# Optimization experiments

Measured on AMD Instinct MI355X. Metric: run time of the kernel, lower is better.

## Reference

```python
import jax, jax.numpy as jnp
import numpy as np

LAMBDA = 25.0
MU = 25.0
NU = 1.0
ALPHA = 0.25
EPS = 1e-4
NUM_MATCHES = (20, 4)


def _cdist(x, y):
    # x: (B, L1, C), y: (B, L2, C) -> (B, L1, L2) euclidean distances
    x2 = jnp.sum(x * x, axis=-1)[..., :, None]
    y2 = jnp.sum(y * y, axis=-1)[..., None, :]
    d2 = x2 + y2 - 2.0 * jnp.einsum('blc,bmc->blm', x, y)
    return jnp.sqrt(jnp.maximum(d2, 0.0))


def _nearest_neighbors(input_maps, candidate_maps, distances, num_matches):
    # For each input location, its nearest candidate; then keep the
    # num_matches input locations with smallest NN distance, in original order.
    nn_dist = jnp.min(distances, axis=-1)    # (B, L1)
    nn_idx = jnp.argmin(distances, axis=-1)  # (B, L1)
    _, sel = jax.lax.top_k(-nn_dist, num_matches)  # (B, M) smallest distances
    sel = jnp.sort(sel, axis=1)  # restore original ordering of positions
    filtered_input = jnp.take_along_axis(input_maps, sel[..., None], axis=1)
    nn_sel = jnp.take_along_axis(nn_idx, sel, axis=1)
    filtered_candidate = jnp.take_along_axis(candidate_maps, nn_sel[..., None], axis=1)
    return filtered_input, filtered_candidate


def _mse(a, b):
    return jnp.mean((a - b) ** 2)


def _vicreg_loss(z_a, z_b):
    inv_loss = _mse(z_a, z_b)

    def var_loss(z):
        std = jnp.sqrt(jnp.var(z, axis=0, ddof=1) + EPS)
        return jnp.mean(jax.nn.relu(1.0 - std))

    def cov_loss(z):
        n, d = z.shape
        zc = z - jnp.mean(z, axis=0)
        cov = (zc.T @ zc) / (n - 1)
        off = cov - jnp.diag(jnp.diag(cov))
        return jnp.sum(off ** 2) / d

    v = 0.5 * (var_loss(z_a) + var_loss(z_b))
    c = cov_loss(z_a) + cov_loss(z_b)
    return LAMBDA * inv_loss + MU * v + NU * c


def _local_loss(z_global, z_local, grid_global, grid_local):
    B = z_global.shape[0]
    zg = z_global.reshape(B, -1, z_global.shape[-1])   # (B, Lg, C)
    zl = z_local.reshape(B, -1, z_local.shape[-1])     # (B, Ll, C)

    inv_loss = 0.0
    # feature-space NN
    gf, gn = _nearest_neighbors(zg, zl, _cdist(zg, zl), NUM_MATCHES[0])
    lf, ln = _nearest_neighbors(zl, zg, _cdist(zl, zg), NUM_MATCHES[1])
    inv_loss = inv_loss + (_mse(gf, gn) / 2 + _mse(lf, ln) / 2)

    # grid-space NN (distances from grids, gather from feature maps)
    gg = grid_global.reshape(B, -1, 2)
    gl = grid_local.reshape(B, -1, 2)
    gf, gn = _nearest_neighbors(zg, zl, _cdist(gg, gl), NUM_MATCHES[0])
    lf, ln = _nearest_neighbors(zl, zg, _cdist(gl, gg), NUM_MATCHES[1])
    inv_loss = inv_loss + (_mse(gf, gn) / 2 + _mse(lf, ln) / 2)

    return LAMBDA * inv_loss


def setup_inputs() -> dict:
    key = jax.random.key(0)
    ks = jax.random.split(key, 6)
    B, D, C = 32, 8192, 512
    return {
        'z_global': jax.random.normal(ks[0], (B, D), jnp.float32),
        'z_local': jax.random.normal(ks[1], (B, D), jnp.float32),
        'z_global_local_features': jax.random.normal(ks[2], (B, 24, 24, C), jnp.float32),
        'z_local_local_features': jax.random.normal(ks[3], (B, 16, 16, C), jnp.float32),
        'grid_global': jax.random.uniform(ks[4], (B, 24, 24, 2), jnp.float32),
        'grid_local': jax.random.uniform(ks[5], (B, 16, 16, 2), jnp.float32),
    }


def reference(z_global, z_local, z_global_local_features, z_local_local_features, grid_global, grid_local):
    global_loss = _vicreg_loss(z_global, z_local)
    local_loss = _local_loss(z_global_local_features, z_local_local_features, grid_global, grid_local)
    return ALPHA * global_loss + (1.0 - ALPHA) * local_loss
```

## Files before the change

kernel.cpp:

```cpp
#include <hip/hip_runtime.h>
#include <hip/hip_bf16.h>

#define BATCH 32
#define DZ    8192
#define LG    576
#define LL    256
#define CH    512

#define OFF_S      0
#define OFF_BSUM   8192
#define OFF_SELSUM 9472
#define OFF_CNT    10496
#define OFF_RNP    10560
#define OFF_CNP    305472
#define WS_NEED    895296

typedef __attribute__((ext_vector_type(8))) short bf16x8;
typedef __attribute__((ext_vector_type(4))) float f32x4;

__device__ __forceinline__ unsigned short f2bf(float x) {
  union { __hip_bfloat16 h; unsigned short u; } cv;
  cv.h = __float2bfloat16(x);
  return cv.u;
}

__device__ __forceinline__ uint4 pack8(float4 lo, float4 hi) {
  union { unsigned short h[8]; uint4 u; } pk;
  pk.h[0] = f2bf(lo.x); pk.h[1] = f2bf(lo.y); pk.h[2] = f2bf(lo.z); pk.h[3] = f2bf(lo.w);
  pk.h[4] = f2bf(hi.x); pk.h[5] = f2bf(hi.y); pk.h[6] = f2bf(hi.z); pk.h[7] = f2bf(hi.w);
  return pk.u;
}

__device__ __forceinline__ float dot4(float4 v) {
  return v.x * v.x + v.y * v.y + v.z * v.z + v.w * v.w;
}

struct SelSmem {
  unsigned long long keys[LG];
  unsigned int nnm[LG];
  float cxy[2 * LG];
  unsigned int plist[40];
  unsigned int cnt;
  float fred[4];
};

template <int V>
__device__ __forceinline__ void sel_case(
    SelSmem& sm, int b,
    const float* __restrict__ zgf, const float* __restrict__ zlf,
    const float* __restrict__ gg, const float* __restrict__ gl,
    const unsigned long long* __restrict__ rowNNp,
    const unsigned long long* __restrict__ colNNp,
    double* __restrict__ selsum) {
  constexpr bool GDIR = (V == 0 || V == 2);
  constexpr int L1 = GDIR ? LG : LL;
  constexpr int L2 = GDIR ? LL : LG;
  constexpr int M  = GDIR ? 20 : 4;
  constexpr int NR = (L1 + 255) / 256;
  const float* fin  = GDIR ? zgf + (size_t)b * LG * CH : zlf + (size_t)b * LL * CH;
  const float* fcan = GDIR ? zlf + (size_t)b * LL * CH : zgf + (size_t)b * LG * CH;
  int tid = threadIdx.x, lane = tid & 63, wv = tid >> 6;
  if (tid == 0) sm.cnt = 0;

  if constexpr (V < 2) {
    constexpr int P = (V == 0) ? 2 : 9;
    const unsigned long long* src =
        (V == 0) ? rowNNp + (size_t)b * LG * 2 : colNNp + (size_t)b * LL * 9;
    #pragma unroll
    for (int s = 0; s < NR; ++s) {
      int l = tid + s * 256;
      if (l < L1) {
        const unsigned long long* q = src + (size_t)l * P;
        unsigned long long p = q[0];
        #pragma unroll
        for (int u = 1; u < P; ++u) { unsigned long long t2 = q[u]; p = t2 < p ? t2 : p; }
        sm.keys[l] = (p & 0xFFFFFFFF00000000ull) | (unsigned)l;
        sm.nnm[l] = (unsigned)(p & 0xFFFFFFFFu);
      }
    }
  } else {
    const float* gin  = (V == 2) ? gg + (size_t)b * LG * 2 : gl + (size_t)b * LL * 2;
    const float* gcan = (V == 2) ? gl + (size_t)b * LL * 2 : gg + (size_t)b * LG * 2;
    #pragma unroll
    for (int s = 0; s < (2 * L2 + 255) / 256; ++s) {
      int i = tid + s * 256;
      if (i < 2 * L2) sm.cxy[i] = gcan[i];
    }
    __syncthreads();
    float x[NR], y[NR], bd[NR];
    unsigned bi[NR];
    #pragma unroll
    for (int s = 0; s < NR; ++s) {
      int l = tid + s * 256;
      x[s] = (l < L1) ? gin[2 * l] : 0.f;
      y[s] = (l < L1) ? gin[2 * l + 1] : 0.f;
      bd[s] = 3.4e38f; bi[s] = 0;
    }
    const float2* c2 = (const float2*)sm.cxy;
    for (int m2 = 0; m2 < L2; m2 += 8) {
      float2 cc[8];
      #pragma unroll
      for (int u = 0; u < 8; ++u) cc[u] = c2[m2 + u];
      #pragma unroll
      for (int u = 0; u < 8; ++u)
        #pragma unroll
        for (int s = 0; s < NR; ++s) {
          float dx = x[s] - cc[u].x, dy = y[s] - cc[u].y;
          float d2 = dx * dx + dy * dy;
          if (d2 < bd[s]) { bd[s] = d2; bi[s] = (unsigned)(m2 + u); }
        }
    }
    #pragma unroll
    for (int s = 0; s < NR; ++s) {
      int l = tid + s * 256;
      if (l < L1) {
        sm.keys[l] = ((unsigned long long)__float_as_uint(bd[s]) << 32) | (unsigned)l;
        sm.nnm[l] = bi[s];
      }
    }
  }
  __syncthreads();

  unsigned long long myk[NR];
  int rk[NR];
  #pragma unroll
  for (int s = 0; s < NR; ++s) {
    int l = tid + s * 256;
    myk[s] = (l < L1) ? sm.keys[l] : ~0ull;
    rk[s] = 0;
  }
  for (int j = 0; j < L1; j += 8) {
    unsigned long long kk[8];
    #pragma unroll
    for (int u = 0; u < 8; ++u) kk[u] = sm.keys[j + u];
    #pragma unroll
    for (int u = 0; u < 8; ++u)
      #pragma unroll
      for (int s = 0; s < NR; ++s) rk[s] += (kk[u] < myk[s]) ? 1 : 0;
  }
  #pragma unroll
  for (int s = 0; s < NR; ++s) {
    int l = tid + s * 256;
    if (l < L1 && rk[s] < M) {
      unsigned slot = atomicAdd(&sm.cnt, 1u);
      sm.plist[2 * slot] = (unsigned)l;
      sm.plist[2 * slot + 1] = sm.nnm[l];
    }
  }
  __syncthreads();

  float part = 0.f;
  #pragma unroll
  for (int rr = 0; rr < M / 4; ++rr) {
    int r = wv + rr * 4;
    const float4* a4 = (const float4*)(fin + (size_t)sm.plist[2 * r] * CH);
    const float4* c4 = (const float4*)(fcan + (size_t)sm.plist[2 * r + 1] * CH);
    float4 xa = a4[lane * 2], xb = a4[lane * 2 + 1];
    float4 ya = c4[lane * 2], yb = c4[lane * 2 + 1];
    float d0 = xa.x - ya.x, d1 = xa.y - ya.y, d2 = xa.z - ya.z, d3 = xa.w - ya.w;
    float d4 = xb.x - yb.x, d5 = xb.y - yb.y, d6 = xb.z - yb.z, d7 = xb.w - yb.w;
    part += d0 * d0 + d1 * d1 + d2 * d2 + d3 * d3 +
            d4 * d4 + d5 * d5 + d6 * d6 + d7 * d7;
  }
  for (int s = 32; s; s >>= 1) part += __shfl_down(part, s);
  if (lane == 0) sm.fred[wv] = part;
  __syncthreads();
  if (tid == 0)
    selsum[V * 32 + b] = (double)(sm.fred[0] + sm.fred[1] + sm.fred[2] + sm.fred[3]);
}

__global__ __launch_bounds__(256) void k_megaA(
    const float* __restrict__ za, const float* __restrict__ zb,
    const float* __restrict__ zgf, const float* __restrict__ zlf,
    const float* __restrict__ gg, const float* __restrict__ gl,
    double* __restrict__ bsum, float* __restrict__ S,
    unsigned long long* __restrict__ rowNNp, unsigned long long* __restrict__ colNNp,
    double* __restrict__ selsum, unsigned int* __restrict__ cnt) {
  __shared__ __align__(16) char smem[31488];
  int tid = threadIdx.x, lane = tid & 63, wv = tid >> 6;
  int blk = blockIdx.x;

  if (blk < 64) {
    SelSmem& sm = *reinterpret_cast<SelSmem*>(smem);
    int b2 = blk >> 1;
    if (blk & 1) sel_case<3>(sm, b2, zgf, zlf, gg, gl, rowNNp, colNNp, selsum);
    else         sel_case<2>(sm, b2, zgf, zlf, gg, gl, rowNNp, colNNp, selsum);
    return;
  }

  if (blk < 640) {
    int fblk = blk - 64;
    int fs = (fblk & 7) * 72 + (fblk >> 3);
    int b = fs / 18, rr_ = fs % 18;
    int by = rr_ / 9, bx = rr_ % 9;
    int row0 = bx * 64, col0 = by * 128;

    unsigned short (*As0)[40] = (unsigned short(*)[40])smem;
    unsigned short (*Bs0)[40] = (unsigned short(*)[40])(smem + 5120);
    unsigned short (*As1)[40] = (unsigned short(*)[40])(smem + 15360);
    unsigned short (*Bs1)[40] = (unsigned short(*)[40])(smem + 20480);
    float* Asn = (float*)(smem + 30720);
    float* Bsn = (float*)(smem + 30976);

    const int m16 = lane & 15, quad = lane >> 4;
    const int wm = wv >> 1, wn = wv & 1;
    const float* Ag = zgf + ((size_t)(b * LG + row0)) * CH;
    const float* Bg = zlf + ((size_t)(b * LL + col0)) * CH;
    const int sr = tid >> 2, sq = tid & 3;
    const int br = tid >> 1, bq = tid & 1;

    f32x4 acc[2][4] = {};
    float ssA = 0.f, ssB = 0.f;
    float4 a0, a1, b0, b1, b2, b3;

    const float* apb = Ag + (size_t)sr * CH + sq * 8;
    const float* bpb = Bg + (size_t)br * CH + bq * 16;

    a0 = *(const float4*)(apb);     a1 = *(const float4*)(apb + 4);
    b0 = *(const float4*)(bpb);     b1 = *(const float4*)(bpb + 4);
    b2 = *(const float4*)(bpb + 8); b3 = *(const float4*)(bpb + 12);
    *(uint4*)&As0[sr][sq * 8]       = pack8(a0, a1);
    *(uint4*)&Bs0[br][bq * 16]      = pack8(b0, b1);
    *(uint4*)&Bs0[br][bq * 16 + 8]  = pack8(b2, b3);
    ssA += dot4(a0) + dot4(a1);
    ssB += dot4(b0) + dot4(b1) + dot4(b2) + dot4(b3);
    a0 = *(const float4*)(apb + 32);      a1 = *(const float4*)(apb + 36);
    b0 = *(const float4*)(bpb + 32);      b1 = *(const float4*)(bpb + 36);
    b2 = *(const float4*)(bpb + 40);      b3 = *(const float4*)(bpb + 44);
    __syncthreads();

    #pragma unroll
    for (int k = 0; k < 8; ++k) {
      {
        bf16x8 af0 = *(const bf16x8*)&As0[wm * 32 + m16][quad * 8];
        bf16x8 af1 = *(const bf16x8*)&As0[wm * 32 + 16 + m16][quad * 8];
        bf16x8 bfv[4];
        #pragma unroll
        for (int j = 0; j < 4; ++j)
          bfv[j] = *(const bf16x8*)&Bs0[wn * 64 + j * 16 + m16][quad * 8];
        #pragma unroll
        for (int j = 0; j < 4; ++j) {
          acc[0][j] = __builtin_amdgcn_mfma_f32_16x16x32_bf16(af0, bfv[j], acc[0][j], 0, 0, 0);
          acc[1][j] = __builtin_amdgcn_mfma_f32_16x16x32_bf16(af1, bfv[j], acc[1][j], 0, 0, 0);
        }
        *(uint4*)&As1[sr][sq * 8]      = pack8(a0, a1);
        *(uint4*)&Bs1[br][bq * 16]     = pack8(b0, b1);
        *(uint4*)&Bs1[br][bq * 16 + 8] = pack8(b2, b3);
        ssA += dot4(a0) + dot4(a1);
        ssB += dot4(b0) + dot4(b1) + dot4(b2) + dot4(b3);
        if (k < 7) {
          int k0 = (2 * k + 2) * 32;
          a0 = *(const float4*)(apb + k0);      a1 = *(const float4*)(apb + k0 + 4);
          b0 = *(const float4*)(bpb + k0);      b1 = *(const float4*)(bpb + k0 + 4);
          b2 = *(const float4*)(bpb + k0 + 8);  b3 = *(const float4*)(bpb + k0 + 12);
        }
        __syncthreads();
      }
      {
        bf16x8 af0 = *(const bf16x8*)&As1[wm * 32 + m16][quad * 8];
        bf16x8 af1 = *(const bf16x8*)&As1[wm * 32 + 16 + m16][quad * 8];
        bf16x8 bfv[4];
        #pragma unroll
        for (int j = 0; j < 4; ++j)
          bfv[j] = *(const bf16x8*)&Bs1[wn * 64 + j * 16 + m16][quad * 8];
        #pragma unroll
        for (int j = 0; j < 4; ++j) {
          acc[0][j] = __builtin_amdgcn_mfma_f32_16x16x32_bf16(af0, bfv[j], acc[0][j], 0, 0, 0);
          acc[1][j] = __builtin_amdgcn_mfma_f32_16x16x32_bf16(af1, bfv[j], acc[1][j], 0, 0, 0);
        }
        if (k < 7) {
          *(uint4*)&As0[sr][sq * 8]      = pack8(a0, a1);
          *(uint4*)&Bs0[br][bq * 16]     = pack8(b0, b1);
          *(uint4*)&Bs0[br][bq * 16 + 8] = pack8(b2, b3);
          ssA += dot4(a0) + dot4(a1);
          ssB += dot4(b0) + dot4(b1) + dot4(b2) + dot4(b3);
          int k0 = (2 * k + 3) * 32;
          a0 = *(const float4*)(apb + k0);      a1 = *(const float4*)(apb + k0 + 4);
          b0 = *(const float4*)(bpb + k0);      b1 = *(const float4*)(bpb + k0 + 4);
          b2 = *(const float4*)(bpb + k0 + 8);  b3 = *(const float4*)(bpb + k0 + 12);
          __syncthreads();
        }
      }
    }

    ssA += __shfl_xor(ssA, 1); ssA += __shfl_xor(ssA, 2);
    ssB += __shfl_xor(ssB, 1);
    __syncthreads();
    if (sq == 0) Asn[sr] = ssA;
    if (bq == 0) Bsn[br] = ssB;
    __syncthreads();

    float na[2][4], nb[4];
    #pragma unroll
    for (int i = 0; i < 2; ++i)
      #pragma unroll
      for (int r = 0; r < 4; ++r)
        na[i][r] = Asn[wm * 32 + i * 16 + quad * 4 + r];
    #pragma unroll
    for (int j = 0; j < 4; ++j)
      nb[j] = Bsn[wn * 64 + j * 16 + m16];

    #pragma unroll
    for (int i = 0; i < 2; ++i) {
      #pragma unroll
      for (int r = 0; r < 4; ++r) {
        unsigned long long p = ~0ull;
        #pragma unroll
        for (int j = 0; j < 4; ++j) {
          float d = fmaxf(na[i][r] + nb[j] - 2.f * acc[i][j][r], 0.f);
          unsigned c = (unsigned)(col0 + wn * 64 + j * 16 + m16);
          unsigned long long pj = (((unsigned long long)__float_as_uint(d)) << 32) | c;
          p = pj < p ? pj : p;
        }
        #pragma unroll
        for (int s = 1; s < 16; s <<= 1) {
          unsigned long long q = __shfl_xor(p, s);
          p = q < p ? q : p;
        }
        if (m16 == 0)
          rowNNp[((size_t)b * LG + row0 + wm * 32 + i * 16 + quad * 4 + r) * 2 + by] = p;
      }
    }
    #pragma unroll
    for (int j = 0; j < 4; ++j) {
      unsigned long long p = ~0ull;
      #pragma unroll
      for (int i = 0; i < 2; ++i) {
        #pragma unroll
        for (int r = 0; r < 4; ++r) {
          float d = fmaxf(na[i][r] + nb[j] - 2.f * acc[i][j][r], 0.f);
          unsigned rg = (unsigned)(row0 + wm * 32 + i * 16 + quad * 4 + r);
          unsigned long long pr = (((unsigned long long)__float_as_uint(d)) << 32) | rg;
          p = pr < p ? pr : p;
        }
      }
      unsigned long long q = __shfl_xor(p, 16); p = q < p ? q : p;
      q = __shfl_xor(p, 32); p = q < p ? q : p;
      if (quad == 0)
        colNNp[((size_t)b * LL + col0 + wn * 64 + j * 16 + m16) * 9 + bx] = p;
    }
    return;
  }

  if (blk < 1696) {
    float (*sred)[5] = (float(*)[5])smem;
    int e = blk - 640;
    int zi = e >= 528; if (zi) e -= 528;
    const float* z = zi ? zb : za;
    float* Sz = S + zi * 1024;
    int p = 0, rem = e;
    while (rem >= 32 - p) { rem -= 32 - p; ++p; }
    int q = p + rem;
    const float4* zp = (const float4*)(z + (size_t)p * DZ);
    const float4* zq = (const float4*)(z + (size_t)q * DZ);
    float s = 0.f;
    #pragma unroll
    for (int ii = 0; ii < 8; ++ii) {
      int i = tid + ii * 256;
      float4 a = zp[i], bb = zq[i];
      s += a.x * bb.x + a.y * bb.y + a.z * bb.z + a.w * bb.w;
    }
    for (int off = 32; off; off >>= 1) s += __shfl_down(s, off);
    if (lane == 0) sred[wv][0] = s;
    __syncthreads();
    if (tid == 0) {
      float r = sred[0][0] + sred[1][0] + sred[2][0] + sred[3][0];
      Sz[p * 32 + q] = r;
      if (p != q) Sz[q * 32 + p] = r;
    }
    return;
  }

  {
    float (*sred)[5] = (float(*)[5])smem;
    int blkS = blk - 1696;
    if (blkS == 0 && tid == 0) cnt[0] = 0;
    int i = blkS * 256 + tid;
    float sa = 0.f, qa = 0.f, sb = 0.f, qb = 0.f, si = 0.f;
    #pragma unroll 8
    for (int b = 0; b < BATCH; ++b) {
      float va = za[(size_t)b * DZ + i];
      float vb = zb[(size_t)b * DZ + i];
      sa += va; qa += va * va;
      sb += vb; qb += vb * vb;
      float d = va - vb; si += d * d;
    }
    float ssa = qa - sa * sa * (1.f / 32.f);
    float ssb = qb - sb * sb * (1.f / 32.f);
    float v0 = si;
    float v1 = fmaxf(0.f, 1.f - sqrtf(ssa * (1.f / 31.f) + 1e-4f));
    float v2 = fmaxf(0.f, 1.f - sqrtf(ssb * (1.f / 31.f) + 1e-4f));
    float v3 = ssa * ssa, v4 = ssb * ssb;
    for (int off = 32; off; off >>= 1) {
      v0 += __shfl_down(v0, off); v1 += __shfl_down(v1, off);
      v2 += __shfl_down(v2, off); v3 += __shfl_down(v3, off);
      v4 += __shfl_down(v4, off);
    }
    if (lane == 0) {
      sred[wv][0] = v0; sred[wv][1] = v1; sred[wv][2] = v2;
      sred[wv][3] = v3; sred[wv][4] = v4;
    }
    __syncthreads();
    if (tid < 5)
      bsum[blkS * 5 + tid] =
          (double)(sred[0][tid] + sred[1][tid] + sred[2][tid] + sred[3][tid]);
  }
}

struct TailSmem {
  SelSmem sel;
  float t[2][32];
  double sacc[5];
  double smf[4];
  int isLast;
};

__global__ __launch_bounds__(256) void k_tail(
    const float* __restrict__ zgf, const float* __restrict__ zlf,
    const float* __restrict__ gg, const float* __restrict__ gl,
    const unsigned long long* __restrict__ rowNNp,
    const unsigned long long* __restrict__ colNNp,
    double* __restrict__ selsum, const double* __restrict__ bsum,
    const float* __restrict__ S, unsigned int* __restrict__ doneCnt,
    float* __restrict__ out) {
  __shared__ TailSmem ts;
  int tid = threadIdx.x;
  int b = blockIdx.x >> 1, V = blockIdx.x & 1;
  if (V == 0) sel_case<0>(ts.sel, b, zgf, zlf, gg, gl, rowNNp, colNNp, selsum);
  else        sel_case<1>(ts.sel, b, zgf, zlf, gg, gl, rowNNp, colNNp, selsum);

  if (tid == 0) {
    __threadfence();
    unsigned r = atomicAdd(doneCnt, 1u);
    ts.isLast = (r == 63) ? 1 : 0;
  }
  __syncthreads();
  if (!ts.isLast) return;
  __threadfence();

  if (tid < 32) {
    #pragma unroll
    for (int zi = 0; zi < 2; ++zi) {
      float tp = 0.f;
      for (int bb = 0; bb < 32; ++bb) tp += S[zi * 1024 + tid * 32 + bb];
      ts.t[zi][tid] = tp * (1.f / 32.f);
    }
  }
  if (tid < 5) {
    double s = 0.0;
    for (int blk2 = 0; blk2 < 32; ++blk2) s += bsum[blk2 * 5 + tid];
    ts.sacc[tid] = s;
  }
  if (tid >= 8 && tid < 12) {
    int v = tid - 8;
    double s = 0.0;
    for (int bb = 0; bb < 32; ++bb) s += selsum[v * 32 + bb];
    ts.smf[v] = s;
  }
  __syncthreads();
  if (tid < 64) {
    double total[2];
    #pragma unroll
    for (int zi = 0; zi < 2; ++zi) {
      float u = 0.f;
      for (int bb = 0; bb < 32; ++bb) u += ts.t[zi][bb];
      u *= (1.f / 32.f);
      double s = 0.0;
      for (int e2 = tid; e2 < 1024; e2 += 64) {
        int p = e2 >> 5, q = e2 & 31;
        float G = S[zi * 1024 + e2] - ts.t[zi][p] - ts.t[zi][q] + u;
        s += (double)G * (double)G;
      }
      for (int off = 32; off; off >>= 1) s += __shfl_down(s, off);
      total[zi] = s;
    }
    if (tid == 0) {
      double inv_g = ts.sacc[0] / (32.0 * 8192.0);
      double v = 0.5 * (ts.sacc[1] + ts.sacc[2]) / 8192.0;
      double c = (total[0] - ts.sacc[3] + total[1] - ts.sacc[4]) / (961.0 * 8192.0);
      double gloss = 25.0 * inv_g + 25.0 * v + c;
      double mfg = ts.smf[0] / (32.0 * 20.0 * 512.0);
      double mfl = ts.smf[1] / (32.0 * 4.0 * 512.0);
      double mgg = ts.smf[2] / (32.0 * 20.0 * 512.0);
      double mgl = ts.smf[3] / (32.0 * 4.0 * 512.0);
      double lloss = 25.0 * (0.5 * (mfg + mfl) + 0.5 * (mgg + mgl));
      out[0] = (float)(0.25 * gloss + 0.75 * lloss);
    }
  }
}

extern "C" void kernel_launch(void* const* d_in, const int* in_sizes, int n_in,
                              void* d_out, int out_size, void* d_ws, size_t ws_size,
                              hipStream_t stream) {
  const float* zg  = (const float*)d_in[0];
  const float* zl  = (const float*)d_in[1];
  const float* zgf = (const float*)d_in[2];
  const float* zlf = (const float*)d_in[3];
  const float* gg  = (const float*)d_in[4];
  const float* glo = (const float*)d_in[5];

  char* ws = (char*)d_ws;
  float* S       = (float*)(ws + OFF_S);
  double* bsum   = (double*)(ws + OFF_BSUM);
  double* selsum = (double*)(ws + OFF_SELSUM);
  unsigned int* cnt = (unsigned int*)(ws + OFF_CNT);
  unsigned long long* rowNNp = (unsigned long long*)(ws + OFF_RNP);
  unsigned long long* colNNp = (unsigned long long*)(ws + OFF_CNP);

  k_megaA<<<1728, 256, 0, stream>>>(zg, zl, zgf, zlf, gg, glo,
                                    bsum, S, rowNNp, colNNp, selsum, cnt);
  k_tail<<<64, 256, 0, stream>>>(zgf, zlf, gg, glo, rowNNp, colNNp,
                                 selsum, bsum, S, cnt, (float*)d_out);
}
```

Baseline: 137.9 us.

## Fuse per-batch feature-NN selection into distance blocks via last-block counters

The feature-space NN selection (sel_case 0/1) moves out of the separate tail kernel. The last of the 18 distance tiles for each batch, detected with a per-batch atomic counter, now runs both selections inside the main kernel. A tiny single-wave kernel does the final reduction, and a memset resets the counters. This is meant to overlap the selection work with the remaining distance tiles instead of serialising it after a kernel boundary. The cost is an extra memset launch, and the two selections now run serially in one block per batch instead of in two parallel blocks.

```diff
diff --git a/kernel.cpp b/kernel.cpp
--- a/kernel.cpp
+++ b/kernel.cpp
@@ -11,9 +11,9 @@
 #define OFF_BSUM   8192
 #define OFF_SELSUM 9472
 #define OFF_CNT    10496
-#define OFF_RNP    10560
-#define OFF_CNP    305472
-#define WS_NEED    895296
+#define OFF_RNP    10752
+#define OFF_CNP    305664
+#define WS_NEED    895488
 
 typedef __attribute__((ext_vector_type(8))) short bf16x8;
 typedef __attribute__((ext_vector_type(4))) float f32x4;
@@ -169,14 +169,15 @@
     selsum[V * 32 + b] = (double)(sm.fred[0] + sm.fred[1] + sm.fred[2] + sm.fred[3]);
 }
 
-__global__ __launch_bounds__(256) void k_megaA(
+#define FFLAG 31488
+__global__ __launch_bounds__(256) void k_one(
     const float* __restrict__ za, const float* __restrict__ zb,
     const float* __restrict__ zgf, const float* __restrict__ zlf,
     const float* __restrict__ gg, const float* __restrict__ gl,
     double* __restrict__ bsum, float* __restrict__ S,
     unsigned long long* __restrict__ rowNNp, unsigned long long* __restrict__ colNNp,
-    double* __restrict__ selsum, unsigned int* __restrict__ cnt) {
-  __shared__ __align__(16) char smem[31488];
+    double* __restrict__ selsum, unsigned int* __restrict__ cntB) {
+  __shared__ __align__(16) char smem[31504];
   int tid = threadIdx.x, lane = tid & 63, wv = tid >> 6;
   int blk = blockIdx.x;
 
@@ -338,6 +339,21 @@
       q = __shfl_xor(p, 32); p = q < p ? q : p;
       if (quad == 0)
         colNNp[((size_t)b * LL + col0 + wn * 64 + j * 16 + m16) * 9 + bx] = p;
+    }
+
+    __syncthreads();
+    volatile int* fflag = (volatile int*)(smem + FFLAG);
+    if (tid == 0) {
+      __threadfence();
+      unsigned rb = atomicAdd(&cntB[b], 1u);
+      *fflag = (rb == 17u) ? 1 : 0;
+    }
+    __syncthreads();
+    if (*fflag) {
+      __threadfence();
+      SelSmem& sm = *reinterpret_cast<SelSmem*>(smem);
+      sel_case<0>(sm, b, zgf, zlf, gg, gl, rowNNp, colNNp, selsum);
+      sel_case<1>(sm, b, zgf, zlf, gg, gl, rowNNp, colNNp, selsum);
     }
     return;
   }
@@ -374,7 +390,6 @@
   {
     float (*sred)[5] = (float(*)[5])smem;
     int blkS = blk - 1696;
-    if (blkS == 0 && tid == 0) cnt[0] = 0;
     int i = blkS * 256 + tid;
     float sa = 0.f, qa = 0.f, sb = 0.f, qb = 0.f, si = 0.f;
     #pragma unroll 8
@@ -407,85 +422,59 @@
   }
 }
 
-struct TailSmem {
-  SelSmem sel;
-  float t[2][32];
-  double sacc[5];
-  double smf[4];
-  int isLast;
-};
-
-__global__ __launch_bounds__(256) void k_tail(
-    const float* __restrict__ zgf, const float* __restrict__ zlf,
-    const float* __restrict__ gg, const float* __restrict__ gl,
-    const unsigned long long* __restrict__ rowNNp,
-    const unsigned long long* __restrict__ colNNp,
-    double* __restrict__ selsum, const double* __restrict__ bsum,
-    const float* __restrict__ S, unsigned int* __restrict__ doneCnt,
-    float* __restrict__ out) {
-  __shared__ TailSmem ts;
-  int tid = threadIdx.x;
-  int b = blockIdx.x >> 1, V = blockIdx.x & 1;
-  if (V == 0) sel_case<0>(ts.sel, b, zgf, zlf, gg, gl, rowNNp, colNNp, selsum);
-  else        sel_case<1>(ts.sel, b, zgf, zlf, gg, gl, rowNNp, colNNp, selsum);
-
-  if (tid == 0) {
-    __threadfence();
-    unsigned r = atomicAdd(doneCnt, 1u);
-    ts.isLast = (r == 63) ? 1 : 0;
-  }
-  __syncthreads();
-  if (!ts.isLast) return;
-  __threadfence();
-
-  if (tid < 32) {
-    #pragma unroll
-    for (int zi = 0; zi < 2; ++zi) {
+__global__ __launch_bounds__(64) void k_fin(
+    const double* __restrict__ bsum, const double* __restrict__ selsum,
+    const float* __restrict__ S, float* __restrict__ out) {
+  __shared__ float t[2][32];
+  __shared__ double sacc[5];
+  __shared__ double smf[4];
+  int lane = threadIdx.x;
+  #pragma unroll
+  for (int zi = 0; zi < 2; ++zi) {
+    if (lane < 32) {
       float tp = 0.f;
-      for (int bb = 0; bb < 32; ++bb) tp += S[zi * 1024 + tid * 32 + bb];
-      ts.t[zi][tid] = tp * (1.f / 32.f);
-    }
-  }
-  if (tid < 5) {
+      for (int bb = 0; bb < 32; ++bb) tp += S[zi * 1024 + lane * 32 + bb];
+      t[zi][lane] = tp * (1.f / 32.f);
+    }
+  }
+  if (lane < 5) {
     double s = 0.0;
-    for (int blk2 = 0; blk2 < 32; ++blk2) s += bsum[blk2 * 5 + tid];
-    ts.sacc[tid] = s;
-  }
-  if (tid >= 8 && tid < 12) {
-    int v = tid - 8;
+    for (int blk = 0; blk < 32; ++blk) s += bsum[blk * 5 + lane];
+    sacc[lane] = s;
+  }
+  if (lane >= 8 && lane < 12) {
+    int v = lane - 8;
     double s = 0.0;
     for (int bb = 0; bb < 32; ++bb) s += selsum[v * 32 + bb];
-    ts.smf[v] = s;
+    smf[v] = s;
   }
   __syncthreads();
-  if (tid < 64) {
-    double total[2];
-    #pragma unroll
-    for (int zi = 0; zi < 2; ++zi) {
-      float u = 0.f;
-      for (int bb = 0; bb < 32; ++bb) u += ts.t[zi][bb];
-      u *= (1.f / 32.f);
-      double s = 0.0;
-      for (int e2 = tid; e2 < 1024; e2 += 64) {
-        int p = e2 >> 5, q = e2 & 31;
-        float G = S[zi * 1024 + e2] - ts.t[zi][p] - ts.t[zi][q] + u;
-        s += (double)G * (double)G;
-      }
-      for (int off = 32; off; off >>= 1) s += __shfl_down(s, off);
-      total[zi] = s;
-    }
-    if (tid == 0) {
-      double inv_g = ts.sacc[0] / (32.0 * 8192.0);
-      double v = 0.5 * (ts.sacc[1] + ts.sacc[2]) / 8192.0;
-      double c = (total[0] - ts.sacc[3] + total[1] - ts.sacc[4]) / (961.0 * 8192.0);
-      double gloss = 25.0 * inv_g + 25.0 * v + c;
-      double mfg = ts.smf[0] / (32.0 * 20.0 * 512.0);
-      double mfl = ts.smf[1] / (32.0 * 4.0 * 512.0);
-      double mgg = ts.smf[2] / (32.0 * 20.0 * 512.0);
-      double mgl = ts.smf[3] / (32.0 * 4.0 * 512.0);
-      double lloss = 25.0 * (0.5 * (mfg + mfl) + 0.5 * (mgg + mgl));
-      out[0] = (float)(0.25 * gloss + 0.75 * lloss);
-    }
+  double total[2];
+  #pragma unroll
+  for (int zi = 0; zi < 2; ++zi) {
+    float u = 0.f;
+    for (int bb = 0; bb < 32; ++bb) u += t[zi][bb];
+    u *= (1.f / 32.f);
+    double s = 0.0;
+    for (int e = lane; e < 1024; e += 64) {
+      int p = e >> 5, q = e & 31;
+      float G = S[zi * 1024 + e] - t[zi][p] - t[zi][q] + u;
+      s += (double)G * (double)G;
+    }
+    for (int off = 32; off; off >>= 1) s += __shfl_down(s, off);
+    total[zi] = s;
+  }
+  if (lane == 0) {
+    double inv_g = sacc[0] / (32.0 * 8192.0);
+    double v = 0.5 * (sacc[1] + sacc[2]) / 8192.0;
+    double c = (total[0] - sacc[3] + total[1] - sacc[4]) / (961.0 * 8192.0);
+    double gloss = 25.0 * inv_g + 25.0 * v + c;
+    double mfg = smf[0] / (32.0 * 20.0 * 512.0);
+    double mfl = smf[1] / (32.0 * 4.0 * 512.0);
+    double mgg = smf[2] / (32.0 * 20.0 * 512.0);
+    double mgl = smf[3] / (32.0 * 4.0 * 512.0);
+    double lloss = 25.0 * (0.5 * (mfg + mfl) + 0.5 * (mgg + mgl));
+    out[0] = (float)(0.25 * gloss + 0.75 * lloss);
   }
 }
 
@@ -503,12 +492,12 @@
   float* S       = (float*)(ws + OFF_S);
   double* bsum   = (double*)(ws + OFF_BSUM);
   double* selsum = (double*)(ws + OFF_SELSUM);
-  unsigned int* cnt = (unsigned int*)(ws + OFF_CNT);
+  unsigned int* cntB = (unsigned int*)(ws + OFF_CNT);
   unsigned long long* rowNNp = (unsigned long long*)(ws + OFF_RNP);
   unsigned long long* colNNp = (unsigned long long*)(ws + OFF_CNP);
 
-  k_megaA<<<1728, 256, 0, stream>>>(zg, zl, zgf, zlf, gg, glo,
-                                    bsum, S, rowNNp, colNNp, selsum, cnt);
-  k_tail<<<64, 256, 0, stream>>>(zgf, zlf, gg, glo, rowNNp, colNNp,
-                                 selsum, bsum, S, cnt, (float*)d_out);
-}
+  hipMemsetAsync(ws + OFF_CNT, 0, 256, stream);
+  k_one<<<1728, 256, 0, stream>>>(zg, zl, zgf, zlf, gg, glo,
+                                  bsum, S, rowNNp, colNNp, selsum, cntB);
+  k_fin<<<1, 64, 0, stream>>>(bsum, selsum, S, (float*)d_out);
+}
```

New measurement: 172.7 us. 1.25x slower.
